# Optimization experiments

Hardware: AMD Instinct MI355X
Metric: run time of the kernel (lower is better)

## Reference

```python
import jax, jax.numpy as jnp
import numpy as np
import math

# Fixed ChunkedBlockDiagonalMask configuration (int metadata, closed over)
BATCH_SIZES = [32, 16, 8]
SEQ_LENS = [512, 1024, 2048]
NUM_HEADS = 8
HEAD_DIM = 64
TOTAL_TOKENS = sum(b * s for b, s in zip(BATCH_SIZES, SEQ_LENS))  # 49152


def setup_inputs() -> dict:
    key = jax.random.key(0)
    kq, kk, kv = jax.random.split(key, 3)
    shape = (1, NUM_HEADS, TOTAL_TOKENS, HEAD_DIM)
    return {
        "query": jax.random.normal(kq, shape, dtype=jnp.float32),
        "key": jax.random.normal(kk, shape, dtype=jnp.float32),
        "value": jax.random.normal(kv, shape, dtype=jnp.float32),
    }


def _sdpa(q, k, v):
    # q,k,v: [B, H, S, D]; native-backend math: softmax(q k^T / sqrt(D)) v
    scale = 1.0 / math.sqrt(q.shape[-1])
    scores = jnp.einsum("bhqd,bhkd->bhqk", q * scale, k)
    probs = jax.nn.softmax(scores, axis=-1)
    return jnp.einsum("bhqk,bhkd->bhqd", probs, v)


def reference(query, key, value):
    # Packed layout: [1, H, sum_i(B_i*S_i), D]; per-chunk token dim is (B_i S_i)
    H, D = query.shape[1], query.shape[3]
    outs = []
    offset = 0
    for b, s in zip(BATCH_SIZES, SEQ_LENS):
        n = b * s
        def unpack(t):
            # [1,H,(b s),D] -> [b,H,s,D]
            c = t[0, :, offset:offset + n, :]          # [H, b*s, D]
            return c.reshape(H, b, s, D).transpose(1, 0, 2, 3)
        o = _sdpa(unpack(query), unpack(key), unpack(value))  # [b,H,s,D]
        outs.append(o.transpose(1, 0, 2, 3).reshape(1, H, n, D))
        offset += n
    return jnp.concatenate(outs, axis=2)
```

## Files before the change

### kernel.cpp

```cpp
#include <hip/hip_runtime.h>

typedef __bf16 bf16_t;
typedef bf16_t bf16x8 __attribute__((ext_vector_type(8)));
typedef float f32x4 __attribute__((ext_vector_type(4)));
typedef unsigned short u16x8_t __attribute__((ext_vector_type(8)));
typedef unsigned int u32x4_t __attribute__((ext_vector_type(4)));

#define HD 64
#define TOTTOK 49152

__device__ __forceinline__ unsigned short f2b(float f) {
    bf16_t h = (bf16_t)f;
    return __builtin_bit_cast(unsigned short, h);
}
__device__ __forceinline__ bf16x8 asbf(u16x8_t u) { return __builtin_bit_cast(bf16x8, u); }
__device__ __forceinline__ bf16x8 asbf4(u32x4_t u) { return __builtin_bit_cast(bf16x8, u); }

__global__ __launch_bounds__(256, 2)
void flash_attn_kernel(const float* __restrict__ Q, const float* __restrict__ K,
                       const float* __restrict__ V, float* __restrict__ O)
{
    __shared__ unsigned short Kf[2][8][64][8];
    __shared__ unsigned short Vf[2][8][64][8];

    const int bid = blockIdx.x;
    int Slen, bl2, off, qtl2, base;
    if (bid < 512)       { Slen = 2048; bl2 = 3; off = 32768; qtl2 = 3; base = 0;    }
    else if (bid < 1024) { Slen = 1024; bl2 = 4; off = 16384; qtl2 = 2; base = 512;  }
    else                 { Slen = 512;  bl2 = 5; off = 0;     qtl2 = 1; base = 1024; }
    const int l    = bid - base;
    const int xcd  = l & 7;
    const int slot = l >> 3;
    const int p    = xcd + ((slot >> qtl2) << 3);
    const int qt   = slot & ((1 << qtl2) - 1);
    const int hh   = p >> bl2;
    const int sj   = p & ((1 << bl2) - 1);

    const size_t seqbase = ((size_t)hh * TOTTOK + (size_t)off + (size_t)sj * Slen) * HD;
    const float* Qb = Q + seqbase + (size_t)(qt * 256) * HD;
    const float* Kb = K + seqbase;
    const float* Vb = V + seqbase;
    float*       Ob = O + seqbase + (size_t)(qt * 256) * HD;

    const int tid  = threadIdx.x;
    const int wave = tid >> 6;
    const int lane = tid & 63;
    const int lg   = lane >> 4;
    const int li   = lane & 15;
    const bool lam = (lg & 1) != 0;

    const float SC = 0.125f * 1.4426950408889634f;

    bf16x8 qh[4][2];
#pragma unroll
    for (int st = 0; st < 4; ++st)
#pragma unroll
      for (int c = 0; c < 2; ++c) {
        const float* src = Qb + (size_t)(wave*64 + st*16 + li) * HD + c*32 + lg*8;
        float4 a = *(const float4*)src;
        float4 b = *(const float4*)(src + 4);
        float f[8] = {a.x,a.y,a.z,a.w,b.x,b.y,b.z,b.w};
        bf16x8 hi;
#pragma unroll
        for (int i = 0; i < 8; ++i) hi[i] = (bf16_t)(f[i] * SC);
        qh[st][c] = hi;
      }

    f32x4 oacc[4][4];
    float lsum[4];
    float mrow[4];
#pragma unroll
    for (int st = 0; st < 4; ++st) {
      lsum[st] = 0.f; mrow[st] = -1e30f;
#pragma unroll
      for (int t = 0; t < 4; ++t) oacc[st][t] = (f32x4){0.f,0.f,0.f,0.f};
    }

    const int kkey = tid >> 4;
    const int kd   = (tid & 15) * 4;
    const int kch  = (kd >> 5);
    const int klan = kkey + ((kd >> 3) & 3) * 16;
    const int kel  = kd & 7;
    const int vkg  = (tid & 15) * 4;
    const int vdc  = (tid >> 4) * 4;
    const int vch  = (vdc >> 4) * 2 + (vkg >> 5);
    const int vlan = ((vkg >> 3) & 3) * 16 + (vdc & 15);
    const int vel  = vkg & 7;

    float4 kr[4], vr[4];
    auto LOADT = [&](int it) {
      const float* Ksrc = Kb + (size_t)(it * 64) * HD;
      const float* Vsrc = Vb + (size_t)(it * 64) * HD;
#pragma unroll
      for (int i = 0; i < 4; ++i)
        kr[i] = *(const float4*)(Ksrc + (size_t)(kkey + i*16)*HD + kd);
#pragma unroll
      for (int i = 0; i < 4; ++i)
        vr[i] = *(const float4*)(Vsrc + (size_t)(vkg + i)*HD + vdc);
    };
    auto STORET = [&](int buf) {
#pragma unroll
      for (int i = 0; i < 4; ++i) {
        ushort4 u;
        u.x = f2b(kr[i].x); u.y = f2b(kr[i].y); u.z = f2b(kr[i].z); u.w = f2b(kr[i].w);
        *(ushort4*)&Kf[buf][i*2 + kch][klan][kel] = u;
      }
      float vm[4][4];
#pragma unroll
      for (int i = 0; i < 4; ++i) {
        vm[i][0] = vr[i].x; vm[i][1] = vr[i].y; vm[i][2] = vr[i].z; vm[i][3] = vr[i].w;
      }
#pragma unroll
      for (int di = 0; di < 4; ++di) {
        ushort4 u;
        u.x = f2b(vm[0][di]); u.y = f2b(vm[1][di]); u.z = f2b(vm[2][di]); u.w = f2b(vm[3][di]);
        *(ushort4*)&Vf[buf][vch][vlan + di][vel] = u;
      }
    };

    const int niter = Slen >> 6;
    LOADT(0);
    STORET(0);
    __syncthreads();

    for (int it = 0; it < niter; ++it) {
      const int cur = it & 1;
      const bool more = (it + 1 < niter);
      if (more) LOADT(it + 1);

      bf16x8 kf[4][2];
#pragma unroll
      for (int kt = 0; kt < 4; ++kt)
#pragma unroll
        for (int c = 0; c < 2; ++c)
          kf[kt][c] = asbf(*(const u16x8_t*)&Kf[cur][kt*2 + c][lane][0]);

      u32x4_t pb[4][2];
#pragma unroll
      for (int st = 0; st < 4; ++st) {
        f32x4 s[4];
        __builtin_amdgcn_s_setprio(1);
#pragma unroll
        for (int kt = 0; kt < 4; ++kt) {
          f32x4 z = (f32x4){0.f,0.f,0.f,0.f};
          z = __builtin_amdgcn_mfma_f32_16x16x32_bf16(kf[kt][0], qh[st][0], z, 0, 0, 0);
          z = __builtin_amdgcn_mfma_f32_16x16x32_bf16(kf[kt][1], qh[st][1], z, 0, 0, 0);
          s[kt] = z;
        }
        __builtin_amdgcn_s_setprio(0);

        float p01 = fmaxf(fmaxf(s[0][0], s[0][1]), fmaxf(s[0][2], s[0][3]));
        float p23 = fmaxf(fmaxf(s[1][0], s[1][1]), fmaxf(s[1][2], s[1][3]));
        float p45 = fmaxf(fmaxf(s[2][0], s[2][1]), fmaxf(s[2][2], s[2][3]));
        float p67 = fmaxf(fmaxf(s[3][0], s[3][1]), fmaxf(s[3][2], s[3][3]));
        float pmax = fmaxf(fmaxf(p01, p23), fmaxf(p45, p67));
        if (!__all(pmax <= mrow[st] + 8.0f)) {
          float mx = pmax;
          mx = fmaxf(mx, __shfl_xor(mx, 16));
          mx = fmaxf(mx, __shfl_xor(mx, 32));
          float mnew = fmaxf(mrow[st], mx);
          float corr = __builtin_amdgcn_exp2f(mrow[st] - mnew);
          mrow[st] = mnew;
          lsum[st] *= corr;
#pragma unroll
          for (int t = 0; t < 4; ++t) oacc[st][t] *= corr;
        }
        const float m = mrow[st];
        unsigned int W[4][2];
        float ls = 0.f;
#pragma unroll
        for (int kt = 0; kt < 4; ++kt) {
#pragma unroll
          for (int jw = 0; jw < 2; ++jw) {
            float e0 = __builtin_amdgcn_exp2f(s[kt][2*jw]   - m);
            float e1 = __builtin_amdgcn_exp2f(s[kt][2*jw+1] - m);
            ls += e0 + e1;
            W[kt][jw] = (unsigned int)f2b(e0) | ((unsigned int)f2b(e1) << 16);
          }
        }
        lsum[st] += ls;

#pragma unroll
        for (int c = 0; c < 2; ++c) {
          unsigned int a0 = W[2*c][0], b0 = W[2*c+1][0];
          unsigned int a1 = W[2*c][1], b1 = W[2*c+1][1];
          asm("v_permlane32_swap_b32 %0, %1" : "+v"(a0), "+v"(b0));
          asm("v_permlane32_swap_b32 %0, %1" : "+v"(a1), "+v"(b1));
          unsigned int q0 = lam ? a0 : b0;
          unsigned int q1 = lam ? a1 : b1;
          unsigned int s0 = __builtin_amdgcn_ds_swizzle((int)q0, 0x401F);
          unsigned int s1 = __builtin_amdgcn_ds_swizzle((int)q1, 0x401F);
          u32x4_t pw;
          pw[0] = lam ? s0 : a0;
          pw[1] = lam ? s1 : a1;
          pw[2] = lam ? b0 : s0;
          pw[3] = lam ? b1 : s1;
          pb[st][c] = pw;
        }
      }

      __builtin_amdgcn_s_setprio(1);
#pragma unroll
      for (int c = 0; c < 2; ++c) {
#pragma unroll
        for (int t = 0; t < 4; ++t) {
          bf16x8 vb = asbf(*(const u16x8_t*)&Vf[cur][t*2 + c][lane][0]);
          oacc[0][t] = __builtin_amdgcn_mfma_f32_16x16x32_bf16(vb, asbf4(pb[0][c]), oacc[0][t], 0, 0, 0);
          oacc[1][t] = __builtin_amdgcn_mfma_f32_16x16x32_bf16(vb, asbf4(pb[1][c]), oacc[1][t], 0, 0, 0);
          oacc[2][t] = __builtin_amdgcn_mfma_f32_16x16x32_bf16(vb, asbf4(pb[2][c]), oacc[2][t], 0, 0, 0);
          oacc[3][t] = __builtin_amdgcn_mfma_f32_16x16x32_bf16(vb, asbf4(pb[3][c]), oacc[3][t], 0, 0, 0);
        }
      }
      __builtin_amdgcn_s_setprio(0);

      if (more) {
        STORET(cur ^ 1);
        __syncthreads();
      }
    }

#pragma unroll
    for (int st = 0; st < 4; ++st) {
      float ls = lsum[st];
      ls += __shfl_xor(ls, 16);
      ls += __shfl_xor(ls, 32);
      float inv = 1.0f / ls;
      float* dst = Ob + (size_t)(wave*64 + st*16 + li) * HD + lg*4;
#pragma unroll
      for (int t = 0; t < 4; ++t) {
        float4 o4;
        o4.x = oacc[st][t][0] * inv;
        o4.y = oacc[st][t][1] * inv;
        o4.z = oacc[st][t][2] * inv;
        o4.w = oacc[st][t][3] * inv;
        *(float4*)(dst + t*16) = o4;
      }
    }
}

extern "C" void kernel_launch(void* const* d_in, const int* in_sizes, int n_in,
                              void* d_out, int out_size, void* d_ws, size_t ws_size,
                              hipStream_t stream) {
    (void)in_sizes; (void)n_in; (void)out_size; (void)d_ws; (void)ws_size;
    const float* Q = (const float*)d_in[0];
    const float* K = (const float*)d_in[1];
    const float* V = (const float*)d_in[2];
    float* O = (float*)d_out;
    flash_attn_kernel<<<dim3(1536), dim3(256), 0, stream>>>(Q, K, V, O);
}
```

Before: 220.9 us.

## Compute row sums via MFMA with ones, relayout K/V LDS, raise occupancy

Replaces the scalar per-lane softmax row-sum accumulation with an extra MFMA against an all-ones bf16 operand, so the sum comes out already reduced across lanes and no end shuffles are needed. It rewrites the K tile loads to wide 8-element contiguous LDS stores, and stores V in a padded row layout that is read as two 4-element chunks. The launch bound moves to 3 blocks per CU. The row sum is now taken from bf16-rounded probabilities, which changes rounding slightly. The extra MFMAs and tighter register budget at higher occupancy could cost throughput or cause spills.

```diff
diff --git a/kernel.cpp b/kernel.cpp
--- a/kernel.cpp
+++ b/kernel.cpp
@@ -16,12 +16,12 @@
 __device__ __forceinline__ bf16x8 asbf(u16x8_t u) { return __builtin_bit_cast(bf16x8, u); }
 __device__ __forceinline__ bf16x8 asbf4(u32x4_t u) { return __builtin_bit_cast(bf16x8, u); }
 
-__global__ __launch_bounds__(256, 2)
+__global__ __launch_bounds__(256, 3)
 void flash_attn_kernel(const float* __restrict__ Q, const float* __restrict__ K,
                        const float* __restrict__ V, float* __restrict__ O)
 {
-    __shared__ unsigned short Kf[2][8][64][8];
-    __shared__ unsigned short Vf[2][8][64][8];
+    __shared__ unsigned short Kf[2][4096];
+    __shared__ unsigned short Vf[2][4160];
 
     const int bid = blockIdx.x;
     int Slen, bl2, off, qtl2, base;
@@ -67,54 +67,59 @@
       }
 
     f32x4 oacc[4][4];
-    float lsum[4];
+    f32x4 lacc[4];
     float mrow[4];
 #pragma unroll
     for (int st = 0; st < 4; ++st) {
-      lsum[st] = 0.f; mrow[st] = -1e30f;
+      mrow[st] = -1e30f;
+      lacc[st] = (f32x4){0.f,0.f,0.f,0.f};
 #pragma unroll
       for (int t = 0; t < 4; ++t) oacc[st][t] = (f32x4){0.f,0.f,0.f,0.f};
     }
 
-    const int kkey = tid >> 4;
-    const int kd   = (tid & 15) * 4;
-    const int kch  = (kd >> 5);
-    const int klan = kkey + ((kd >> 3) & 3) * 16;
-    const int kel  = kd & 7;
+    u16x8_t onesu;
+#pragma unroll
+    for (int i = 0; i < 8; ++i) onesu[i] = 0x3F80;
+    const bf16x8 ones = asbf(onesu);
+
+    const int krow = ((tid >> 7) & 1) * 16 + (tid & 15);
+    const int kd0  = ((tid >> 6) & 1) * 32 + ((tid >> 4) & 3) * 8;
     const int vkg  = (tid & 15) * 4;
     const int vdc  = (tid >> 4) * 4;
-    const int vch  = (vdc >> 4) * 2 + (vkg >> 5);
-    const int vlan = ((vkg >> 3) & 3) * 16 + (vdc & 15);
-    const int vel  = vkg & 7;
-
-    float4 kr[4], vr[4];
+
+    float4 kr0, kr1, kr2, kr3, vr[4];
     auto LOADT = [&](int it) {
       const float* Ksrc = Kb + (size_t)(it * 64) * HD;
       const float* Vsrc = Vb + (size_t)(it * 64) * HD;
+      kr0 = *(const float4*)(Ksrc + (size_t)krow * HD + kd0);
+      kr1 = *(const float4*)(Ksrc + (size_t)krow * HD + kd0 + 4);
+      kr2 = *(const float4*)(Ksrc + (size_t)(krow + 32) * HD + kd0);
+      kr3 = *(const float4*)(Ksrc + (size_t)(krow + 32) * HD + kd0 + 4);
 #pragma unroll
       for (int i = 0; i < 4; ++i)
-        kr[i] = *(const float4*)(Ksrc + (size_t)(kkey + i*16)*HD + kd);
-#pragma unroll
-      for (int i = 0; i < 4; ++i)
-        vr[i] = *(const float4*)(Vsrc + (size_t)(vkg + i)*HD + vdc);
+        vr[i] = *(const float4*)(Vsrc + (size_t)(vkg + i) * HD + vdc);
     };
     auto STORET = [&](int buf) {
-#pragma unroll
-      for (int i = 0; i < 4; ++i) {
-        ushort4 u;
-        u.x = f2b(kr[i].x); u.y = f2b(kr[i].y); u.z = f2b(kr[i].z); u.w = f2b(kr[i].w);
-        *(ushort4*)&Kf[buf][i*2 + kch][klan][kel] = u;
-      }
+      unsigned short* kdst = &Kf[buf][0];
+      u16x8_t a;
+      a[0]=f2b(kr0.x); a[1]=f2b(kr0.y); a[2]=f2b(kr0.z); a[3]=f2b(kr0.w);
+      a[4]=f2b(kr1.x); a[5]=f2b(kr1.y); a[6]=f2b(kr1.z); a[7]=f2b(kr1.w);
+      *(u16x8_t*)(kdst + tid*8) = a;
+      a[0]=f2b(kr2.x); a[1]=f2b(kr2.y); a[2]=f2b(kr2.z); a[3]=f2b(kr2.w);
+      a[4]=f2b(kr3.x); a[5]=f2b(kr3.y); a[6]=f2b(kr3.z); a[7]=f2b(kr3.w);
+      *(u16x8_t*)(kdst + 2048 + tid*8) = a;
+
       float vm[4][4];
 #pragma unroll
       for (int i = 0; i < 4; ++i) {
         vm[i][0] = vr[i].x; vm[i][1] = vr[i].y; vm[i][2] = vr[i].z; vm[i][3] = vr[i].w;
       }
-#pragma unroll
-      for (int di = 0; di < 4; ++di) {
+      char* vdst = (char*)&Vf[buf][0] + (vkg >> 2) * 520;
+#pragma unroll
+      for (int j = 0; j < 4; ++j) {
         ushort4 u;
-        u.x = f2b(vm[0][di]); u.y = f2b(vm[1][di]); u.z = f2b(vm[2][di]); u.w = f2b(vm[3][di]);
-        *(ushort4*)&Vf[buf][vch][vlan + di][vel] = u;
+        u.x = f2b(vm[0][j]); u.y = f2b(vm[1][j]); u.z = f2b(vm[2][j]); u.w = f2b(vm[3][j]);
+        *(ushort4*)(vdst + (vdc + j) * 8) = u;
       }
     };
 
@@ -133,7 +138,7 @@
       for (int kt = 0; kt < 4; ++kt)
 #pragma unroll
         for (int c = 0; c < 2; ++c)
-          kf[kt][c] = asbf(*(const u16x8_t*)&Kf[cur][kt*2 + c][lane][0]);
+          kf[kt][c] = asbf(*(const u16x8_t*)&Kf[cur][(kt*2 + c)*512 + lane*8]);
 
       u32x4_t pb[4][2];
 #pragma unroll
@@ -161,25 +166,21 @@
           float mnew = fmaxf(mrow[st], mx);
           float corr = __builtin_amdgcn_exp2f(mrow[st] - mnew);
           mrow[st] = mnew;
-          lsum[st] *= corr;
+          lacc[st] *= corr;
 #pragma unroll
           for (int t = 0; t < 4; ++t) oacc[st][t] *= corr;
         }
         const float m = mrow[st];
         unsigned int W[4][2];
-        float ls = 0.f;
 #pragma unroll
         for (int kt = 0; kt < 4; ++kt) {
 #pragma unroll
           for (int jw = 0; jw < 2; ++jw) {
             float e0 = __builtin_amdgcn_exp2f(s[kt][2*jw]   - m);
             float e1 = __builtin_amdgcn_exp2f(s[kt][2*jw+1] - m);
-            ls += e0 + e1;
             W[kt][jw] = (unsigned int)f2b(e0) | ((unsigned int)f2b(e1) << 16);
           }
         }
-        lsum[st] += ls;
-
 #pragma unroll
         for (int c = 0; c < 2; ++c) {
           unsigned int a0 = W[2*c][0], b0 = W[2*c+1][0];
@@ -199,16 +200,28 @@
         }
       }
 
+      const char* vrb = (const char*)&Vf[cur][0] + (lane >> 4) * 1040 + (lane & 15) * 8;
       __builtin_amdgcn_s_setprio(1);
 #pragma unroll
       for (int c = 0; c < 2; ++c) {
+        bf16x8 pbf[4];
+#pragma unroll
+        for (int st = 0; st < 4; ++st) {
+          pbf[st] = asbf4(pb[st][c]);
+          lacc[st] = __builtin_amdgcn_mfma_f32_16x16x32_bf16(ones, pbf[st], lacc[st], 0, 0, 0);
+        }
 #pragma unroll
         for (int t = 0; t < 4; ++t) {
-          bf16x8 vb = asbf(*(const u16x8_t*)&Vf[cur][t*2 + c][lane][0]);
-          oacc[0][t] = __builtin_amdgcn_mfma_f32_16x16x32_bf16(vb, asbf4(pb[0][c]), oacc[0][t], 0, 0, 0);
-          oacc[1][t] = __builtin_amdgcn_mfma_f32_16x16x32_bf16(vb, asbf4(pb[1][c]), oacc[1][t], 0, 0, 0);
-          oacc[2][t] = __builtin_amdgcn_mfma_f32_16x16x32_bf16(vb, asbf4(pb[2][c]), oacc[2][t], 0, 0, 0);
-          oacc[3][t] = __builtin_amdgcn_mfma_f32_16x16x32_bf16(vb, asbf4(pb[3][c]), oacc[3][t], 0, 0, 0);
+          ushort4 lo4 = *(const ushort4*)(vrb + (c*8 + 0)*520 + t*128);
+          ushort4 hi4 = *(const ushort4*)(vrb + (c*8 + 1)*520 + t*128);
+          u16x8_t vv;
+          vv[0]=lo4.x; vv[1]=lo4.y; vv[2]=lo4.z; vv[3]=lo4.w;
+          vv[4]=hi4.x; vv[5]=hi4.y; vv[6]=hi4.z; vv[7]=hi4.w;
+          bf16x8 vbf = asbf(vv);
+          oacc[0][t] = __builtin_amdgcn_mfma_f32_16x16x32_bf16(vbf, pbf[0], oacc[0][t], 0, 0, 0);
+          oacc[1][t] = __builtin_amdgcn_mfma_f32_16x16x32_bf16(vbf, pbf[1], oacc[1][t], 0, 0, 0);
+          oacc[2][t] = __builtin_amdgcn_mfma_f32_16x16x32_bf16(vbf, pbf[2], oacc[2][t], 0, 0, 0);
+          oacc[3][t] = __builtin_amdgcn_mfma_f32_16x16x32_bf16(vbf, pbf[3], oacc[3][t], 0, 0, 0);
         }
       }
       __builtin_amdgcn_s_setprio(0);
@@ -221,10 +234,7 @@
 
 #pragma unroll
     for (int st = 0; st < 4; ++st) {
-      float ls = lsum[st];
-      ls += __shfl_xor(ls, 16);
-      ls += __shfl_xor(ls, 32);
-      float inv = 1.0f / ls;
+      float inv = 1.0f / lacc[st][0];
       float* dst = Ob + (size_t)(wave*64 + st*16 + li) * HD + lg*4;
 #pragma unroll
       for (int t = 0; t < 4; ++t) {
```

Result: slower. 769.7 us (+248.5%).
